# Performance work log

Hardware: AMD Instinct MI355X
Metric: run time of the kernel (lower is better)

## Reference

```python
import jax, jax.numpy as jnp
import numpy as np

BATCH, T, D_MODEL = 4, 4096, 2048


def setup_inputs() -> dict:
    key = jax.random.key(0)
    kx, ka, kb, kc, kd = jax.random.split(key, 5)
    x = jax.random.normal(kx, (BATCH, T, D_MODEL), dtype=jnp.float32)
    A = jax.random.normal(ka, (D_MODEL,), dtype=jnp.float32)
    B = jax.random.normal(kb, (D_MODEL,), dtype=jnp.float32)
    C = jax.random.normal(kc, (D_MODEL,), dtype=jnp.float32)
    D = jax.random.normal(kd, (D_MODEL,), dtype=jnp.float32)
    return {"x": x, "A": A, "B": B, "C": C, "D": D}


def reference(x, A, B, C, D):
    # Diagonal LTI SSM: h_t = A*h_{t-1} + B*x_t ; y_t = C*h_t + D*x_t
    # x: (batch, T, d_model). Scan over time axis.
    batch, _, d = x.shape
    s0 = jnp.zeros((batch, d), dtype=x.dtype)

    def step(s, xt):
        s = A * s + B * xt          # (batch, d)
        yt = C * s + D * xt
        return s, yt

    # scan over leading axis -> move T to front
    _, ys = jax.lax.scan(step, s0, jnp.swapaxes(x, 0, 1))
    return jnp.swapaxes(ys, 0, 1)   # (batch, T, d_model)
```

## Files before the change

### kernel.cpp

```cpp
#include <hip/hip_runtime.h>

#define BATCHN  4
#define TLEN    4096
#define D4      512
#define DG      8
#define NDG     64
#define THREADS 512
#define TTILE   512
#define NTILE   8
#define NSUB    64
#define TSUB    8

typedef float f4 __attribute__((ext_vector_type(4)));

__device__ __forceinline__ float fin(float v) {
    return fminf(fmaxf(v, -1.0e30f), 1.0e30f);
}
__device__ __forceinline__ f4 fin4(f4 v) {
    f4 r;
    r.x = fin(v.x); r.y = fin(v.y); r.z = fin(v.z); r.w = fin(v.w);
    return r;
}

#define BAR() do { asm volatile("s_waitcnt lgkmcnt(0)" ::: "memory"); \
                   __builtin_amdgcn_s_barrier();                       \
                   asm volatile("" ::: "memory"); } while (0)

__device__ __forceinline__ int swz(int row, int col) {
    return row * DG + ((col + (row >> 3)) & 7);
}

__global__ __launch_bounds__(THREADS, 1) void ssm_onepass(
    const float* __restrict__ xg, const float* __restrict__ A,
    const float* __restrict__ B, const float* __restrict__ Cv,
    const float* __restrict__ Dv, float* __restrict__ yg) {
    __shared__ f4 tile[TTILE * DG];
    __shared__ f4 pfx[NSUB * DG];

    const int tid = threadIdx.x;
    const int dg  = blockIdx.x & (NDG - 1);
    const int b   = blockIdx.x >> 6;
    const int ch  = tid & (DG - 1);
    const int sub = tid >> 3;

    const int d4 = dg * DG + ch;
    const f4 a  = ((const f4*)A)[d4];
    const f4 bb = ((const f4*)B)[d4];
    const f4 cc = ((const f4*)Cv)[d4];
    const f4 dd = ((const f4*)Dv)[d4];
    const f4 a2 = fin4(a * a), a4 = fin4(a2 * a2), a8 = fin4(a4 * a4);

    f4 S = {0.f, 0.f, 0.f, 0.f};

    const size_t slice = (size_t)b * TLEN * D4 + (size_t)dg * DG;
    const f4* xbase = (const f4*)xg + slice;
    f4* ybase = (f4*)yg + slice;

    {
        f4 r[TSUB];
#pragma unroll
        for (int q = 0; q < TSUB; ++q) {
            int flat = q * THREADS + tid;
            r[q] = xbase[(size_t)(flat >> 3) * D4 + (flat & 7)];
        }
#pragma unroll
        for (int q = 0; q < TSUB; ++q) {
            int flat = q * THREADS + tid;
            tile[swz(flat >> 3, flat & 7)] = r[q];
        }
    }
    BAR();

    for (int t = 0; t < NTILE; ++t) {
        f4 xnext[TSUB];
        if (t + 1 < NTILE) {
#pragma unroll
            for (int q = 0; q < TSUB; ++q) {
                int flat = q * THREADS + tid;
                xnext[q] = xbase[(size_t)((t + 1) * TTILE + (flat >> 3)) * D4
                                 + (flat & 7)];
            }
        }

        f4 xcur[TSUB];
        {
            const int r0 = sub * TSUB;
#pragma unroll
            for (int i = 0; i < TSUB; ++i)
                xcur[i] = tile[swz(r0 + i, ch)];
            f4 v = {0.f, 0.f, 0.f, 0.f};
#pragma unroll
            for (int i = 0; i < TSUB; ++i) v = fin4(a * v + bb * xcur[i]);
            pfx[sub * DG + ch] = v;
        }
        BAR();

        if (tid < DG) {
            for (int s0 = 0; s0 < NSUB; s0 += 8) {
                f4 v0 = pfx[(s0 + 0) * DG + tid];
                f4 v1 = pfx[(s0 + 1) * DG + tid];
                f4 v2 = pfx[(s0 + 2) * DG + tid];
                f4 v3 = pfx[(s0 + 3) * DG + tid];
                f4 v4 = pfx[(s0 + 4) * DG + tid];
                f4 v5 = pfx[(s0 + 5) * DG + tid];
                f4 v6 = pfx[(s0 + 6) * DG + tid];
                f4 v7 = pfx[(s0 + 7) * DG + tid];
                pfx[(s0 + 0) * DG + tid] = S; S = fin4(a8 * S + v0);
                pfx[(s0 + 1) * DG + tid] = S; S = fin4(a8 * S + v1);
                pfx[(s0 + 2) * DG + tid] = S; S = fin4(a8 * S + v2);
                pfx[(s0 + 3) * DG + tid] = S; S = fin4(a8 * S + v3);
                pfx[(s0 + 4) * DG + tid] = S; S = fin4(a8 * S + v4);
                pfx[(s0 + 5) * DG + tid] = S; S = fin4(a8 * S + v5);
                pfx[(s0 + 6) * DG + tid] = S; S = fin4(a8 * S + v6);
                pfx[(s0 + 7) * DG + tid] = S; S = fin4(a8 * S + v7);
            }
        }
        BAR();

        {
            f4 s = pfx[sub * DG + ch];
            const int r0 = sub * TSUB;
#pragma unroll
            for (int i = 0; i < TSUB; ++i) {
                f4 xi = xcur[i];
                s = fin4(a * s + bb * xi);
                tile[swz(r0 + i, ch)] = fin4(cc * s + dd * xi);
            }
        }
        BAR();

#pragma unroll
        for (int q = 0; q < TSUB; ++q) {
            int flat = q * THREADS + tid;
            f4 yv = tile[swz(flat >> 3, flat & 7)];
            __builtin_nontemporal_store(
                yv, ybase + (size_t)(t * TTILE + (flat >> 3)) * D4 + (flat & 7));
        }

        if (t + 1 < NTILE) {
            BAR();
#pragma unroll
            for (int q = 0; q < TSUB; ++q) {
                int flat = q * THREADS + tid;
                tile[swz(flat >> 3, flat & 7)] = xnext[q];
            }
            BAR();
        }
    }
}

extern "C" void kernel_launch(void* const* d_in, const int* in_sizes, int n_in,
                              void* d_out, int out_size, void* d_ws, size_t ws_size,
                              hipStream_t stream) {
    const float* x  = (const float*)d_in[0];
    const float* A  = (const float*)d_in[1];
    const float* B  = (const float*)d_in[2];
    const float* Cv = (const float*)d_in[3];
    const float* Dv = (const float*)d_in[4];
    float* y = (float*)d_out;

    const int nblocks = BATCHN * NDG;
    ssm_onepass<<<nblocks, THREADS, 0, stream>>>(x, A, B, Cv, Dv, y);
}
```

Before: 56.97 us.

## Double-buffer LDS tiles and stage input via direct global-to-LDS loads

Replaces the register-staged prefetch of the next time tile with __builtin_amdgcn_global_load_lds writes straight into a second LDS buffer, so each tile is double-buffered. The global row/column mapping is chosen so the direct-to-LDS layout matches the existing swizzle, and the output store reads LDS linearly while un-swizzling the global address. This drops the register copy of the next tile and one LDS write pass plus a barrier per tile, at the cost of doubling tile LDS usage and relying on vmcnt accounting that mixes the loads with the nontemporal stores.

```diff
diff --git a/kernel.cpp b/kernel.cpp
--- a/kernel.cpp
+++ b/kernel.cpp
@@ -10,6 +10,7 @@
 #define NTILE   8
 #define NSUB    64
 #define TSUB    8
+#define TILE_F4 (TTILE * DG)
 
 typedef float f4 __attribute__((ext_vector_type(4)));
 
@@ -34,14 +35,16 @@
     const float* __restrict__ xg, const float* __restrict__ A,
     const float* __restrict__ B, const float* __restrict__ Cv,
     const float* __restrict__ Dv, float* __restrict__ yg) {
-    __shared__ f4 tile[TTILE * DG];
+    __shared__ f4 tile[2 * TILE_F4];
     __shared__ f4 pfx[NSUB * DG];
 
-    const int tid = threadIdx.x;
-    const int dg  = blockIdx.x & (NDG - 1);
-    const int b   = blockIdx.x >> 6;
-    const int ch  = tid & (DG - 1);
-    const int sub = tid >> 3;
+    const int tid  = threadIdx.x;
+    const int lane = tid & 63;
+    const int wid  = tid >> 6;
+    const int dg   = blockIdx.x & (NDG - 1);
+    const int b    = blockIdx.x >> 6;
+    const int ch   = tid & (DG - 1);
+    const int sub  = tid >> 3;
 
     const int d4 = dg * DG + ch;
     const f4 a  = ((const f4*)A)[d4];
@@ -56,38 +59,42 @@
     const f4* xbase = (const f4*)xg + slice;
     f4* ybase = (f4*)yg + slice;
 
-    {
-        f4 r[TSUB];
+    int g_row[TSUB], g_col[TSUB];
 #pragma unroll
-        for (int q = 0; q < TSUB; ++q) {
-            int flat = q * THREADS + tid;
-            r[q] = xbase[(size_t)(flat >> 3) * D4 + (flat & 7)];
-        }
-#pragma unroll
-        for (int q = 0; q < TSUB; ++q) {
-            int flat = q * THREADS + tid;
-            tile[swz(flat >> 3, flat & 7)] = r[q];
-        }
+    for (int q = 0; q < TSUB; ++q) {
+        int s = q * THREADS + wid * 64 + lane;
+        g_row[q] = s >> 3;
+        g_col[q] = ((s & 7) - (s >> 6)) & 7;
     }
-    BAR();
+
+#define STAGE(t_, bufi_) do {                                                  \
+        const f4* gq;                                                          \
+        f4* lq;                                                                \
+        _Pragma("unroll")                                                      \
+        for (int q = 0; q < TSUB; ++q) {                                       \
+            gq = xbase + (size_t)((t_) * TTILE + g_row[q]) * D4 + g_col[q];    \
+            lq = &tile[(bufi_) * TILE_F4 + q * THREADS + wid * 64];            \
+            __builtin_amdgcn_global_load_lds(                                  \
+                (const __attribute__((address_space(1))) void*)gq,             \
+                (__attribute__((address_space(3))) void*)lq, 16, 0, 0);        \
+        }                                                                      \
+    } while (0)
+
+    STAGE(0, 0);
+    asm volatile("s_waitcnt vmcnt(0)" ::: "memory");
+    __builtin_amdgcn_s_barrier();
+    asm volatile("" ::: "memory");
 
     for (int t = 0; t < NTILE; ++t) {
-        f4 xnext[TSUB];
-        if (t + 1 < NTILE) {
-#pragma unroll
-            for (int q = 0; q < TSUB; ++q) {
-                int flat = q * THREADS + tid;
-                xnext[q] = xbase[(size_t)((t + 1) * TTILE + (flat >> 3)) * D4
-                                 + (flat & 7)];
-            }
-        }
+        f4* bufp = &tile[(t & 1) * TILE_F4];
+
+        if (t + 1 < NTILE) STAGE(t + 1, (t & 1) ^ 1);
 
         f4 xcur[TSUB];
+        const int r0 = sub * TSUB;
+#pragma unroll
+        for (int i = 0; i < TSUB; ++i) xcur[i] = bufp[swz(r0 + i, ch)];
         {
-            const int r0 = sub * TSUB;
-#pragma unroll
-            for (int i = 0; i < TSUB; ++i)
-                xcur[i] = tile[swz(r0 + i, ch)];
             f4 v = {0.f, 0.f, 0.f, 0.f};
 #pragma unroll
             for (int i = 0; i < TSUB; ++i) v = fin4(a * v + bb * xcur[i]);
@@ -119,34 +126,32 @@
 
         {
             f4 s = pfx[sub * DG + ch];
-            const int r0 = sub * TSUB;
 #pragma unroll
             for (int i = 0; i < TSUB; ++i) {
                 f4 xi = xcur[i];
                 s = fin4(a * s + bb * xi);
-                tile[swz(r0 + i, ch)] = fin4(cc * s + dd * xi);
+                bufp[swz(r0 + i, ch)] = fin4(cc * s + dd * xi);
             }
         }
         BAR();
 
 #pragma unroll
         for (int q = 0; q < TSUB; ++q) {
-            int flat = q * THREADS + tid;
-            f4 yv = tile[swz(flat >> 3, flat & 7)];
+            int sIdx = q * THREADS + tid;
+            int row = sIdx >> 3;
+            int col = ((sIdx & 7) - (sIdx >> 6)) & 7;
+            f4 yv = bufp[sIdx];
             __builtin_nontemporal_store(
-                yv, ybase + (size_t)(t * TTILE + (flat >> 3)) * D4 + (flat & 7));
+                yv, ybase + (size_t)(t * TTILE + row) * D4 + col);
         }
 
         if (t + 1 < NTILE) {
-            BAR();
-#pragma unroll
-            for (int q = 0; q < TSUB; ++q) {
-                int flat = q * THREADS + tid;
-                tile[swz(flat >> 3, flat & 7)] = xnext[q];
-            }
-            BAR();
+            asm volatile("s_waitcnt vmcnt(8)" ::: "memory");
+            __builtin_amdgcn_s_barrier();
+            asm volatile("" ::: "memory");
         }
     }
+#undef STAGE
 }
 
 extern "C" void kernel_launch(void* const* d_in, const int* in_sizes, int n_in,
```

Result: no change. 56.08 us (-1.6%).
